# Kernel optimization log

Hardware: AMD Instinct MI355X
Metric: run time of the kernel (lower is better)

## Reference

```python
import jax, jax.numpy as jnp
import numpy as np

INPUT_SIZE = 32   # activity vocab
HIDDEN = 512
OUT = 33          # OUT-1 activity logits + 1 duration
COND = 128
LAYERS = 2
MAXLEN = 64
BATCH = 256
SOS = 0
SLOPE = 0.01      # LeakyReLU default negative slope

def _leaky(x):
    return jnp.where(x >= 0, x, SLOPE * x)

def setup_inputs() -> dict:
    key = jax.random.key(0)
    ks = jax.random.split(key, 16)
    s = 0.05  # small init scale keeps gates in a sane range
    return {
        "batch_size": BATCH,
        "h0": jax.random.normal(ks[0], (LAYERS, BATCH, HIDDEN), jnp.float32),
        "c0": jax.random.normal(ks[1], (LAYERS, BATCH, HIDDEN), jnp.float32),
        "conditionals": jax.random.normal(ks[2], (BATCH, COND), jnp.float32),
        "emb": jax.random.normal(ks[3], (INPUT_SIZE, HIDDEN - 1), jnp.float32) * s,
        "Wih": jax.random.normal(ks[4], (LAYERS, 4 * HIDDEN, HIDDEN), jnp.float32) * s,
        "Whh": jax.random.normal(ks[5], (LAYERS, 4 * HIDDEN, HIDDEN), jnp.float32) * s,
        "bih": jax.random.normal(ks[6], (LAYERS, 4 * HIDDEN), jnp.float32) * s,
        "bhh": jax.random.normal(ks[7], (LAYERS, 4 * HIDDEN), jnp.float32) * s,
        "fcW": jax.random.normal(ks[8], (HIDDEN, COND), jnp.float32) * s,
        "fcb": jax.random.normal(ks[9], (HIDDEN,), jnp.float32) * s,
        "fc2W": jax.random.normal(ks[10], (HIDDEN, HIDDEN), jnp.float32) * s,
        "fc2b": jax.random.normal(ks[11], (HIDDEN,), jnp.float32) * s,
        "fc3W": jax.random.normal(ks[12], (OUT, HIDDEN), jnp.float32) * s,
        "fc3b": jax.random.normal(ks[13], (OUT,), jnp.float32) * s,
    }

def reference(batch_size, h0, c0, conditionals, emb, Wih, Whh, bih, bhh,
              fcW, fcb, fc2W, fc2b, fc3W, fc3b):
    B = h0.shape[1]
    # conditionals branch is step-invariant: compute once (same math as per-step fc+LeakyReLU)
    cond = _leaky(conditionals @ fcW.T + fcb)  # [B, H]
    # decoder_input = zeros[B,1,2] with act channel = sos
    inp0 = jnp.concatenate(
        [jnp.full((B, 1), float(SOS), jnp.float32), jnp.zeros((B, 1), jnp.float32)], axis=-1)

    def step(carry, _):
        h, c, inp = carry  # h,c: [L,B,H], inp: [B,2]
        # CustomDurationEmbedding: embed act index, concat duration channel -> [B,H]
        x = jnp.concatenate([emb[inp[:, 0].astype(jnp.int32)], inp[:, 1:]], axis=-1)
        hs, cs = [], []
        for l in range(LAYERS):  # seq_len==1 per step -> one LSTM cell per layer
            g = x @ Wih[l].T + bih[l] + h[l] @ Whh[l].T + bhh[l]  # [B,4H]
            i_g, f_g, g_g, o_g = jnp.split(g, 4, axis=-1)         # torch gate order i,f,g,o
            c_l = jax.nn.sigmoid(f_g) * c[l] + jax.nn.sigmoid(i_g) * jnp.tanh(g_g)
            h_l = jax.nn.sigmoid(o_g) * jnp.tanh(c_l)
            hs.append(h_l); cs.append(c_l)
            x = h_l
        h_new, c_new = jnp.stack(hs), jnp.stack(cs)
        # conditional_add: (lstm_out + cond) -> fc2 -> LeakyReLU -> fc3
        pred = _leaky((x + cond) @ fc2W.T + fc2b) @ fc3W.T + fc3b  # [B,OUT]
        # pack: topk(1) over activity logits; softmax over singleton seq dim == 1.0
        act = jnp.argmax(pred[:, :OUT - 1], axis=-1).astype(pred.dtype)[:, None]
        dur = jnp.ones((B, 1), pred.dtype)
        nxt = jnp.concatenate([act, dur], axis=-1)
        return (h_new, c_new, nxt), pred

    _, outs = jax.lax.scan(step, (h0, c0, inp0), None, length=MAXLEN)  # [T,B,OUT]
    outs = jnp.transpose(outs, (1, 0, 2))  # [B,T,OUT]
    acts_log_probs = jax.nn.log_softmax(outs[..., :OUT - 1], axis=-1)
    durations = jax.nn.softmax(outs[..., OUT - 1:], axis=1)  # Softmax(dim=-2): over time
    return jnp.concatenate([acts_log_probs, durations], axis=-1)
```

## Files before the change

kernel.cpp:

```cpp
#include <hip/hip_runtime.h>
#include <math.h>

#define BB   256
#define HH   512
#define TT   64
#define NOUT 33
#define CD   128
#define NTHR 1024
#define NWG  256
#define LOFF (4*HH*HH)
#define SZ   (HH*BB)
#define FC2OFF 4194304

typedef float f16v __attribute__((ext_vector_type(16)));
typedef float f8v  __attribute__((ext_vector_type(8)));
typedef const __attribute__((address_space(4))) float cfloat;
typedef const __attribute__((address_space(4))) f16v  cf16v;
typedef const __attribute__((address_space(4))) f8v   cf8v;

__device__ __forceinline__ float sigm(float x)  { return 1.0f/(1.0f+expf(-x)); }
__device__ __forceinline__ float lrelu(float x) { return x >= 0.0f ? x : 0.01f*x; }

__device__ __forceinline__ float gld(const float* p) {
  return __hip_atomic_load(p, __ATOMIC_RELAXED, __HIP_MEMORY_SCOPE_AGENT);
}
__device__ __forceinline__ float2 gld2(const float* p) {
  unsigned long long v = __hip_atomic_load((const unsigned long long*)p,
                                           __ATOMIC_RELAXED, __HIP_MEMORY_SCOPE_AGENT);
  union { unsigned long long u; float2 f; } c; c.u = v; return c.f;
}
__device__ __forceinline__ void gst(float* p, float v) {
  __hip_atomic_store(p, v, __ATOMIC_RELAXED, __HIP_MEMORY_SCOPE_AGENT);
}
__device__ __forceinline__ unsigned gldu(const unsigned* p) {
  return __hip_atomic_load(p, __ATOMIC_RELAXED, __HIP_MEMORY_SCOPE_AGENT);
}

__device__ __forceinline__ cfloat* cptr(const float* p) {
  unsigned long long u = (unsigned long long)p;
  unsigned lo = __builtin_amdgcn_readfirstlane((unsigned)u);
  unsigned hi = __builtin_amdgcn_readfirstlane((unsigned)(u >> 32));
  return (cfloat*)((((unsigned long long)hi) << 32) | (unsigned long long)lo);
}

__device__ __forceinline__ void gbar(unsigned* bar, unsigned ep, int grp, bool fence) {
  __syncthreads();
  if (threadIdx.x == 0) {
    if (fence) __builtin_amdgcn_fence(__ATOMIC_RELEASE, "agent");
    unsigned old = __hip_atomic_fetch_add(&bar[grp*16], 1u, __ATOMIC_RELAXED, __HIP_MEMORY_SCOPE_AGENT);
    if (old == ep*32u + 31u) {
      unsigned o2 = __hip_atomic_fetch_add(&bar[128], 1u, __ATOMIC_RELAXED, __HIP_MEMORY_SCOPE_AGENT);
      if (o2 == ep*8u + 7u)
        __hip_atomic_store(&bar[144], ep+1u, __ATOMIC_RELAXED, __HIP_MEMORY_SCOPE_AGENT);
    }
    while (gldu(&bar[144]) < ep+1u) __builtin_amdgcn_s_sleep(1);
    if (fence) __builtin_amdgcn_fence(__ATOMIC_ACQUIRE, "agent");
  }
  __syncthreads();
}

extern "C" __global__ void __launch_bounds__(256)
transpose_weights(const float* __restrict__ Wih, const float* __restrict__ Whh,
                  const float* __restrict__ fc2W, float* __restrict__ wsT)
{
  const int i = blockIdx.x, tid = threadIdx.x;
  float* dst = wsT + (size_t)i*32768;
  #pragma unroll 1
  for (int idx = tid; idx < 32768; idx += 256) {
    int slot = idx & 31, k = (idx>>5)&511, l = idx>>14;
    int a = slot>>4, r = slot&15, u = r>>2, g = r&3;
    int hu = i*4 + u;
    const float* src = a ? Whh : Wih;
    dst[idx] = src[(size_t)l*LOFF + (size_t)(g*HH+hu)*HH + k];
  }
  float* dstf = wsT + FC2OFF + (size_t)i*2048;
  #pragma unroll 1
  for (int idx = tid; idx < 2048; idx += 256) {
    int r = idx & 3, k = idx >> 2;
    dstf[idx] = fc2W[(size_t)(i*4+r)*HH + k];
  }
}

__device__ __forceinline__ void lstm_phase(const float* __restrict__ wTl,
    const float* __restrict__ bias, float* __restrict__ red,
    const float* __restrict__ xsrc, const float* __restrict__ hsrc,
    float* __restrict__ hdst, float& creg, int i, int j, int tid)
{
  const int lane = tid & 63, ks = tid >> 6;
  cf16v* wp = (cf16v*)cptr(wTl + (size_t)(ks*32)*32);
  const int bo = j*128 + 2*lane;
  const float* xp = xsrc + (size_t)(ks*32)*BB + bo;
  const float* hp = hsrc + (size_t)(ks*32)*BB + bo;

  float acc[32];
  #pragma unroll
  for (int r = 0; r < 32; ++r) acc[r] = 0.f;

  float2 qx0, qh0, qx1, qh1, nx0, nh0, nx1, nh1;
  qx0 = gld2(xp);      qh0 = gld2(hp);
  qx1 = gld2(xp + BB); qh1 = gld2(hp + BB);

  #pragma unroll 1
  for (int it = 0; it < 16; ++it) {
    if (it+1 < 16) {
      nx0 = gld2(xp + (2*it+2)*BB); nh0 = gld2(hp + (2*it+2)*BB);
      nx1 = gld2(xp + (2*it+3)*BB); nh1 = gld2(hp + (2*it+3)*BB);
    }
    {
      f16v wi = wp[it*4+0], wh = wp[it*4+1];
      #pragma unroll
      for (int r = 0; r < 16; ++r) {
        acc[2*r]   += wi[r]*qx0.x + wh[r]*qh0.x;
        acc[2*r+1] += wi[r]*qx0.y + wh[r]*qh0.y;
      }
    }
    {
      f16v wi = wp[it*4+2], wh = wp[it*4+3];
      #pragma unroll
      for (int r = 0; r < 16; ++r) {
        acc[2*r]   += wi[r]*qx1.x + wh[r]*qh1.x;
        acc[2*r+1] += wi[r]*qx1.y + wh[r]*qh1.y;
      }
    }
    qx0 = nx0; qh0 = nh0; qx1 = nx1; qh1 = nh1;
  }
  #pragma unroll
  for (int r = 0; r < 16; ++r)
    *(float2*)(red + (size_t)(ks*16 + r)*128 + 2*lane) = make_float2(acc[2*r], acc[2*r+1]);
  __syncthreads();
  if (tid < 512) {
    const int lhu = tid >> 7, b = tid & 127;
    float g4[4];
    #pragma unroll
    for (int gg = 0; gg < 4; ++gg) {
      float s = bias[lhu*4+gg];
      #pragma unroll
      for (int q = 0; q < 16; ++q) s += red[(size_t)(q*16 + lhu*4+gg)*128 + b];
      g4[gg] = s;
    }
    float ig=sigm(g4[0]), fg=sigm(g4[1]), gv=tanhf(g4[2]), og=sigm(g4[3]);
    float cn = fg*creg + ig*gv;
    creg = cn;
    gst(hdst + (size_t)(i*4+lhu)*BB + j*128 + b, og*tanhf(cn));
  }
}

__device__ __forceinline__ void fc2_phase(const float* __restrict__ h2src,
    const float* __restrict__ wsTf, float* __restrict__ yb,
    const float* lds_bc, const float* condY_l, float* __restrict__ red,
    int i, int j, int tid)
{
  const int lane = tid & 63, ks = tid >> 6;
  cf8v* wpf = (cf8v*)cptr(wsTf + (size_t)ks*128);
  const int bo = j*128 + 2*lane;
  const float* hp = h2src + (size_t)(ks*32)*BB + bo;
  float acc[8];
  #pragma unroll
  for (int r = 0; r < 8; ++r) acc[r] = 0.f;
  float2 qh0, qh1, nh0, nh1;
  qh0 = gld2(hp); qh1 = gld2(hp + BB);
  #pragma unroll 1
  for (int it = 0; it < 16; ++it) {
    if (it+1 < 16) {
      nh0 = gld2(hp + (2*it+2)*BB);
      nh1 = gld2(hp + (2*it+3)*BB);
    }
    f8v w = wpf[it];
    #pragma unroll
    for (int r = 0; r < 4; ++r) {
      acc[2*r]   += w[r]*qh0.x + w[4+r]*qh1.x;
      acc[2*r+1] += w[r]*qh0.y + w[4+r]*qh1.y;
    }
    qh0 = nh0; qh1 = nh1;
  }
  #pragma unroll
  for (int r = 0; r < 4; ++r)
    *(float2*)(red + (size_t)(ks*4+r)*128 + 2*lane) = make_float2(acc[2*r], acc[2*r+1]);
  __syncthreads();
  if (tid < 512) {
    int r = tid >> 7, b = tid & 127;
    float s = lds_bc[r] + condY_l[r*128+b];
    #pragma unroll
    for (int q = 0; q < 16; ++q) s += red[(size_t)(q*4+r)*128 + b];
    gst(yb + (size_t)(i*4+r)*BB + j*128 + b, lrelu(s));
  }
}

extern "C" __global__ void __launch_bounds__(NTHR)
decoder_kernel(const float* __restrict__ h0, const float* __restrict__ c0,
               const float* __restrict__ conds, const float* __restrict__ emb,
               const float* __restrict__ wsTW, const float* __restrict__ bih,
               const float* __restrict__ bhh, const float* __restrict__ fcW,
               const float* __restrict__ fcb, const float* __restrict__ fc2W,
               const float* __restrict__ fc2b, const float* __restrict__ fc3W,
               const float* __restrict__ fc3b,
               float* __restrict__ out, unsigned* bar, float* wsf)
{
  const int w = blockIdx.x;
  const int i = w & 127, j = w >> 7;
  const int grp = w & 7;
  const int tid = threadIdx.x;

  float* xbuf  = wsf;
  float* h1a = wsf + 1*SZ;  float* h1b = wsf + 2*SZ;
  float* h2a = wsf + 3*SZ;  float* h2b = wsf + 4*SZ;
  float* yb  = wsf + 5*SZ;
  float* condb = wsf + 6*SZ;
  const float* wTi  = wsTW + (size_t)i*32768;
  const float* wsTf = wsTW + FC2OFF + (size_t)i*2048;

  __shared__ float red[32768];
  __shared__ float lds_y[HH];
  __shared__ float part[NOUT][17];
  __shared__ float condY_l[512];
  __shared__ float lds_b1[16], lds_b2[16], lds_bc[4];
  __shared__ int   lds_act;

  if (tid < 16) {
    int u2 = tid >> 2, g = tid & 3;
    int hu = i*4 + u2;
    lds_b1[tid] = bih[g*HH+hu] + bhh[g*HH+hu];
    lds_b2[tid] = bih[4*HH + g*HH+hu] + bhh[4*HH + g*HH+hu];
  }
  if (tid < 4) lds_bc[tid] = fc2b[i*4 + tid];

  {
    int u = tid >> 8, b = tid & 255;
    int hug = i*4 + u;
    h1a[(size_t)hug*BB + b] = h0[(size_t)b*HH + hug];
    h2a[(size_t)hug*BB + b] = h0[(size_t)(BB+b)*HH + hug];
    xbuf[(size_t)hug*BB + b] = (hug < HH-1) ? emb[hug] : 0.0f;
    const float* crow = conds + (size_t)b*CD;
    cfloat* fr = cptr(fcW + (size_t)hug*CD);
    float s = fcb[hug];
    #pragma unroll 4
    for (int q = 0; q < CD; q += 4)
      s += fr[q]*crow[q] + fr[q+1]*crow[q+1] + fr[q+2]*crow[q+2] + fr[q+3]*crow[q+3];
    condb[(size_t)hug*BB + b] = lrelu(s);
  }
  float c1 = 0.f, c2 = 0.f;
  if (tid < 512) {
    int lhu = tid >> 7, b = tid & 127;
    int hug = i*4 + lhu, bg = j*128 + b;
    c1 = c0[(size_t)bg*HH + hug];
    c2 = c0[(size_t)(BB+bg)*HH + hug];
  }
  unsigned ep = 0;
  gbar(bar, ep++, grp, true);

  if (tid < 512) {
    int r = tid >> 7, b = tid & 127, bg = j*128 + b;
    cfloat* wr = cptr(fc2W + (size_t)(i*4+r)*HH);
    float s = 0.f;
    #pragma unroll 4
    for (int k = 0; k < HH; ++k) s += wr[k]*condb[(size_t)k*BB + bg];
    condY_l[r*128 + b] = s;
  }
  __syncthreads();

  for (int t = 0; t < TT; ++t) {
    float* h1r = (t&1) ? h1b : h1a;  float* h1w = (t&1) ? h1a : h1b;
    float* h2r = (t&1) ? h2b : h2a;  float* h2w = (t&1) ? h2a : h2b;

    lstm_phase(wTi,         lds_b1, red, xbuf, h1r, h1w, c1, i, j, tid);
    gbar(bar, ep++, grp, false);
    lstm_phase(wTi + 16384, lds_b2, red, h1w, h2r, h2w, c2, i, j, tid);
    gbar(bar, ep++, grp, false);
    fc2_phase(h2w, wsTf, yb, lds_bc, condY_l, red, i, j, tid);
    gbar(bar, ep++, grp, false);
    {
      if (tid < 512) lds_y[tid] = gld(yb + (size_t)tid*BB + w);
      __syncthreads();
      int o = 0, kc = 0;
      bool active = false;
      if (tid < 512)      { o = tid & 31; kc = tid >> 5; active = true; }
      else if (tid < 528) { o = 32;       kc = tid - 512; active = true; }
      if (active) {
        float p = 0.f;
        const float* fw = fc3W + (size_t)o*HH + kc*32;
        #pragma unroll
        for (int k2 = 0; k2 < 32; ++k2) p += fw[k2] * lds_y[kc*32 + k2];
        part[o][kc] = p;
      }
      __syncthreads();
      float predv = -1e30f;
      if (tid < NOUT) {
        float s = fc3b[tid];
        #pragma unroll
        for (int kc2 = 0; kc2 < 16; ++kc2) s += part[tid][kc2];
        predv = s;
        out[(size_t)(w*TT + t)*NOUT + tid] = s;
      }
      if (tid < 64) {
        float v  = (tid < 32) ? predv : -1e30f;
        int  idx = tid;
        #pragma unroll
        for (int off = 32; off > 0; off >>= 1) {
          float ov = __shfl_xor(v, off);
          int   oi = __shfl_xor(idx, off);
          if (ov > v || (ov == v && oi < idx)) { v = ov; idx = oi; }
        }
        if (tid == 0) lds_act = idx;
      }
      __syncthreads();
      const int act = lds_act;
      if (tid < 512)
        gst(xbuf + (size_t)tid*BB + w, (tid < HH-1) ? emb[(size_t)act*(HH-1) + tid] : 1.0f);
    }
    gbar(bar, ep++, grp, false);
  }

  if (tid < TT) {
    const int s = tid;
    float* po = out + (size_t)(w*TT + s)*NOUT;
    float v[NOUT];
    #pragma unroll
    for (int o = 0; o < NOUT; ++o) v[o] = po[o];
    float m = v[0];
    #pragma unroll
    for (int o = 1; o < 32; ++o) m = fmaxf(m, v[o]);
    float sum = 0.f;
    #pragma unroll
    for (int o = 0; o < 32; ++o) sum += expf(v[o] - m);
    float lse = m + logf(sum);
    #pragma unroll
    for (int o = 0; o < 32; ++o) po[o] = v[o] - lse;
    float d = v[32];
    float dm = d;
    #pragma unroll
    for (int off = 32; off > 0; off >>= 1) dm = fmaxf(dm, __shfl_xor(dm, off));
    float e = expf(d - dm);
    float es = e;
    #pragma unroll
    for (int off = 32; off > 0; off >>= 1) es += __shfl_xor(es, off);
    po[32] = e / es;
  }
}

extern "C" void kernel_launch(void* const* d_in, const int* in_sizes, int n_in,
                              void* d_out, int out_size, void* d_ws, size_t ws_size,
                              hipStream_t stream) {
  const float* h0   = (const float*)d_in[1];
  const float* c0   = (const float*)d_in[2];
  const float* cnd  = (const float*)d_in[3];
  const float* emb  = (const float*)d_in[4];
  const float* Wih  = (const float*)d_in[5];
  const float* Whh  = (const float*)d_in[6];
  const float* bih  = (const float*)d_in[7];
  const float* bhh  = (const float*)d_in[8];
  const float* fcW  = (const float*)d_in[9];
  const float* fcb  = (const float*)d_in[10];
  const float* fc2W = (const float*)d_in[11];
  const float* fc2b = (const float*)d_in[12];
  const float* fc3W = (const float*)d_in[13];
  const float* fc3b = (const float*)d_in[14];

  unsigned* bar = (unsigned*)d_ws;
  float* wsf = (float*)((char*)d_ws + 1024);
  float* wsT = wsf + 7*SZ;

  (void)hipMemsetAsync(d_ws, 0, 1024, stream);

  hipLaunchKernelGGL(transpose_weights, dim3(128), dim3(256), 0, stream,
                     Wih, Whh, fc2W, wsT);
  hipLaunchKernelGGL(decoder_kernel, dim3(NWG), dim3(NTHR), 0, stream,
                     h0, c0, cnd, emb, wsT, bih, bhh, fcW, fcb,
                     fc2W, fc2b, fc3W, fc3b, (float*)d_out, bar, wsf);
}
```

Before: 4.062 ms.

## Split batch across 512 workgroups with independent per-batch-slice grid barriers

Doubles the persistent grid to 512 workgroups, each handling 64 batch columns instead of 128. The grid barrier becomes per batch quarter, so the four batch slices synchronise independently because batch rows never interact. Only half of the workgroups now run the fc3, argmax and embedding step, each for its own batch row. LSTM and fc2 inner loops switch from paired float2 loads to scalar loads with double-buffered prefetch, and gate accumulation goes through an extra LDS buffer. In exchange, each weight slice is read twice as often, and the persistent barrier scheme only works if two 1024-thread workgroups fit on each CU at the same time.

```diff
diff --git a/kernel.cpp b/kernel.cpp
--- a/kernel.cpp
+++ b/kernel.cpp
@@ -7,27 +7,20 @@
 #define NOUT 33
 #define CD   128
 #define NTHR 1024
-#define NWG  256
+#define NWG  512
 #define LOFF (4*HH*HH)
 #define SZ   (HH*BB)
 #define FC2OFF 4194304
 
 typedef float f16v __attribute__((ext_vector_type(16)));
-typedef float f8v  __attribute__((ext_vector_type(8)));
 typedef const __attribute__((address_space(4))) float cfloat;
 typedef const __attribute__((address_space(4))) f16v  cf16v;
-typedef const __attribute__((address_space(4))) f8v   cf8v;
 
 __device__ __forceinline__ float sigm(float x)  { return 1.0f/(1.0f+expf(-x)); }
 __device__ __forceinline__ float lrelu(float x) { return x >= 0.0f ? x : 0.01f*x; }
 
 __device__ __forceinline__ float gld(const float* p) {
   return __hip_atomic_load(p, __ATOMIC_RELAXED, __HIP_MEMORY_SCOPE_AGENT);
-}
-__device__ __forceinline__ float2 gld2(const float* p) {
-  unsigned long long v = __hip_atomic_load((const unsigned long long*)p,
-                                           __ATOMIC_RELAXED, __HIP_MEMORY_SCOPE_AGENT);
-  union { unsigned long long u; float2 f; } c; c.u = v; return c.f;
 }
 __device__ __forceinline__ void gst(float* p, float v) {
   __hip_atomic_store(p, v, __ATOMIC_RELAXED, __HIP_MEMORY_SCOPE_AGENT);
@@ -43,17 +36,17 @@
   return (cfloat*)((((unsigned long long)hi) << 32) | (unsigned long long)lo);
 }
 
-__device__ __forceinline__ void gbar(unsigned* bar, unsigned ep, int grp, bool fence) {
+__device__ __forceinline__ void gbar(unsigned* bar, unsigned ep, int j, int sg, bool fence) {
   __syncthreads();
   if (threadIdx.x == 0) {
     if (fence) __builtin_amdgcn_fence(__ATOMIC_RELEASE, "agent");
-    unsigned old = __hip_atomic_fetch_add(&bar[grp*16], 1u, __ATOMIC_RELAXED, __HIP_MEMORY_SCOPE_AGENT);
+    unsigned old = __hip_atomic_fetch_add(&bar[(j*4+sg)*16], 1u, __ATOMIC_RELAXED, __HIP_MEMORY_SCOPE_AGENT);
     if (old == ep*32u + 31u) {
-      unsigned o2 = __hip_atomic_fetch_add(&bar[128], 1u, __ATOMIC_RELAXED, __HIP_MEMORY_SCOPE_AGENT);
-      if (o2 == ep*8u + 7u)
-        __hip_atomic_store(&bar[144], ep+1u, __ATOMIC_RELAXED, __HIP_MEMORY_SCOPE_AGENT);
-    }
-    while (gldu(&bar[144]) < ep+1u) __builtin_amdgcn_s_sleep(1);
+      unsigned o2 = __hip_atomic_fetch_add(&bar[256 + j*16], 1u, __ATOMIC_RELAXED, __HIP_MEMORY_SCOPE_AGENT);
+      if (o2 == ep*4u + 3u)
+        __hip_atomic_store(&bar[320 + j*16], ep+1u, __ATOMIC_RELAXED, __HIP_MEMORY_SCOPE_AGENT);
+    }
+    while (gldu(&bar[320 + j*16]) < ep+1u) __builtin_amdgcn_s_sleep(1);
     if (fence) __builtin_amdgcn_fence(__ATOMIC_ACQUIRE, "agent");
   }
   __syncthreads();
@@ -82,66 +75,66 @@
 }
 
 __device__ __forceinline__ void lstm_phase(const float* __restrict__ wTl,
-    const float* __restrict__ bias, float* __restrict__ red,
+    const float* __restrict__ bias, float* __restrict__ red, float* __restrict__ gbuf,
     const float* __restrict__ xsrc, const float* __restrict__ hsrc,
     float* __restrict__ hdst, float& creg, int i, int j, int tid)
 {
   const int lane = tid & 63, ks = tid >> 6;
   cf16v* wp = (cf16v*)cptr(wTl + (size_t)(ks*32)*32);
-  const int bo = j*128 + 2*lane;
+  const int bo = j*64 + lane;
   const float* xp = xsrc + (size_t)(ks*32)*BB + bo;
   const float* hp = hsrc + (size_t)(ks*32)*BB + bo;
 
-  float acc[32];
-  #pragma unroll
-  for (int r = 0; r < 32; ++r) acc[r] = 0.f;
-
-  float2 qx0, qh0, qx1, qh1, nx0, nh0, nx1, nh1;
-  qx0 = gld2(xp);      qh0 = gld2(hp);
-  qx1 = gld2(xp + BB); qh1 = gld2(hp + BB);
-
-  #pragma unroll 1
-  for (int it = 0; it < 16; ++it) {
-    if (it+1 < 16) {
-      nx0 = gld2(xp + (2*it+2)*BB); nh0 = gld2(hp + (2*it+2)*BB);
-      nx1 = gld2(xp + (2*it+3)*BB); nh1 = gld2(hp + (2*it+3)*BB);
-    }
-    {
-      f16v wi = wp[it*4+0], wh = wp[it*4+1];
+  float acc[16];
+  #pragma unroll
+  for (int r = 0; r < 16; ++r) acc[r] = 0.f;
+
+  float qA[16], qB[16];
+  #pragma unroll
+  for (int kk = 0; kk < 8; ++kk) {
+    qA[kk*2]   = gld(xp + kk*BB);
+    qA[kk*2+1] = gld(hp + kk*BB);
+  }
+  #pragma unroll
+  for (int c = 0; c < 4; ++c) {
+    float* q = (c & 1) ? qB : qA;
+    float* p = (c & 1) ? qA : qB;
+    if (c < 3) {
       #pragma unroll
-      for (int r = 0; r < 16; ++r) {
-        acc[2*r]   += wi[r]*qx0.x + wh[r]*qh0.x;
-        acc[2*r+1] += wi[r]*qx0.y + wh[r]*qh0.y;
-      }
-    }
-    {
-      f16v wi = wp[it*4+2], wh = wp[it*4+3];
+      for (int kk = 0; kk < 8; ++kk) {
+        p[kk*2]   = gld(xp + (c*8+8+kk)*BB);
+        p[kk*2+1] = gld(hp + (c*8+8+kk)*BB);
+      }
+    }
+    #pragma unroll
+    for (int kk = 0; kk < 8; ++kk) {
+      f16v wi = wp[(c*8+kk)*2];
+      f16v wh = wp[(c*8+kk)*2+1];
+      float xv = q[kk*2], hv = q[kk*2+1];
       #pragma unroll
-      for (int r = 0; r < 16; ++r) {
-        acc[2*r]   += wi[r]*qx1.x + wh[r]*qh1.x;
-        acc[2*r+1] += wi[r]*qx1.y + wh[r]*qh1.y;
-      }
-    }
-    qx0 = nx0; qh0 = nh0; qx1 = nx1; qh1 = nh1;
-  }
-  #pragma unroll
-  for (int r = 0; r < 16; ++r)
-    *(float2*)(red + (size_t)(ks*16 + r)*128 + 2*lane) = make_float2(acc[2*r], acc[2*r+1]);
-  __syncthreads();
-  if (tid < 512) {
-    const int lhu = tid >> 7, b = tid & 127;
-    float g4[4];
-    #pragma unroll
-    for (int gg = 0; gg < 4; ++gg) {
-      float s = bias[lhu*4+gg];
-      #pragma unroll
-      for (int q = 0; q < 16; ++q) s += red[(size_t)(q*16 + lhu*4+gg)*128 + b];
-      g4[gg] = s;
-    }
-    float ig=sigm(g4[0]), fg=sigm(g4[1]), gv=tanhf(g4[2]), og=sigm(g4[3]);
-    float cn = fg*creg + ig*gv;
+      for (int r = 0; r < 16; ++r) acc[r] += wi[r]*xv + wh[r]*hv;
+    }
+  }
+  #pragma unroll
+  for (int r = 0; r < 16; ++r) red[(size_t)(ks*16 + r)*64 + lane] = acc[r];
+  __syncthreads();
+  {
+    const int row = tid >> 6, b = tid & 63;
+    float s = bias[row];
+    #pragma unroll
+    for (int q = 0; q < 16; ++q) s += red[(size_t)(q*16 + row)*64 + b];
+    gbuf[row*64 + b] = s;
+  }
+  __syncthreads();
+  if (tid < 256) {
+    const int lhu = tid >> 6, b = tid & 63;
+    float i_g = sigm(gbuf[(lhu*4+0)*64 + b]);
+    float f_g = sigm(gbuf[(lhu*4+1)*64 + b]);
+    float g_g = tanhf(gbuf[(lhu*4+2)*64 + b]);
+    float o_g = sigm(gbuf[(lhu*4+3)*64 + b]);
+    float cn = f_g*creg + i_g*g_g;
     creg = cn;
-    gst(hdst + (size_t)(i*4+lhu)*BB + j*128 + b, og*tanhf(cn));
+    gst(hdst + (size_t)(i*4+lhu)*BB + j*64 + b, o_g*tanhf(cn));
   }
 }
 
@@ -151,38 +144,41 @@
     int i, int j, int tid)
 {
   const int lane = tid & 63, ks = tid >> 6;
-  cf8v* wpf = (cf8v*)cptr(wsTf + (size_t)ks*128);
-  const int bo = j*128 + 2*lane;
+  cf16v* wp = (cf16v*)cptr(wsTf + (size_t)(ks*32)*4);
+  const int bo = j*64 + lane;
   const float* hp = h2src + (size_t)(ks*32)*BB + bo;
-  float acc[8];
-  #pragma unroll
-  for (int r = 0; r < 8; ++r) acc[r] = 0.f;
-  float2 qh0, qh1, nh0, nh1;
-  qh0 = gld2(hp); qh1 = gld2(hp + BB);
-  #pragma unroll 1
-  for (int it = 0; it < 16; ++it) {
-    if (it+1 < 16) {
-      nh0 = gld2(hp + (2*it+2)*BB);
-      nh1 = gld2(hp + (2*it+3)*BB);
-    }
-    f8v w = wpf[it];
-    #pragma unroll
-    for (int r = 0; r < 4; ++r) {
-      acc[2*r]   += w[r]*qh0.x + w[4+r]*qh1.x;
-      acc[2*r+1] += w[r]*qh0.y + w[4+r]*qh1.y;
-    }
-    qh0 = nh0; qh1 = nh1;
-  }
-  #pragma unroll
-  for (int r = 0; r < 4; ++r)
-    *(float2*)(red + (size_t)(ks*4+r)*128 + 2*lane) = make_float2(acc[2*r], acc[2*r+1]);
-  __syncthreads();
-  if (tid < 512) {
-    int r = tid >> 7, b = tid & 127;
-    float s = lds_bc[r] + condY_l[r*128+b];
-    #pragma unroll
-    for (int q = 0; q < 16; ++q) s += red[(size_t)(q*4+r)*128 + b];
-    gst(yb + (size_t)(i*4+r)*BB + j*128 + b, lrelu(s));
+  float acc[4] = {0.f, 0.f, 0.f, 0.f};
+  float qA[8], qB[8];
+  #pragma unroll
+  for (int kk = 0; kk < 8; ++kk) qA[kk] = gld(hp + kk*BB);
+  #pragma unroll
+  for (int c = 0; c < 4; ++c) {
+    float* q = (c & 1) ? qB : qA;
+    float* p = (c & 1) ? qA : qB;
+    if (c < 3) {
+      #pragma unroll
+      for (int kk = 0; kk < 8; ++kk) p[kk] = gld(hp + (c*8+8+kk)*BB);
+    }
+    #pragma unroll
+    for (int kk2 = 0; kk2 < 2; ++kk2) {
+      f16v wv = wp[c*2 + kk2];
+      #pragma unroll
+      for (int k4 = 0; k4 < 4; ++k4) {
+        float hv = q[kk2*4 + k4];
+        #pragma unroll
+        for (int r = 0; r < 4; ++r) acc[r] += wv[k4*4 + r]*hv;
+      }
+    }
+  }
+  #pragma unroll
+  for (int r = 0; r < 4; ++r) red[(size_t)(ks*4 + r)*64 + lane] = acc[r];
+  __syncthreads();
+  if (tid < 256) {
+    const int r = tid >> 6, b = tid & 63;
+    float s = lds_bc[r] + condY_l[r*64 + b];
+    #pragma unroll
+    for (int q = 0; q < 16; ++q) s += red[(size_t)(q*4 + r)*64 + b];
+    gst(yb + (size_t)(i*4+r)*BB + j*64 + b, lrelu(s));
   }
 }
 
@@ -198,10 +194,10 @@
 {
   const int w = blockIdx.x;
   const int i = w & 127, j = w >> 7;
-  const int grp = w & 7;
+  const int sg = (i >> 5) & 3;
   const int tid = threadIdx.x;
 
-  float* xbuf  = wsf;
+  float* xbuf = wsf;
   float* h1a = wsf + 1*SZ;  float* h1b = wsf + 2*SZ;
   float* h2a = wsf + 3*SZ;  float* h2b = wsf + 4*SZ;
   float* yb  = wsf + 5*SZ;
@@ -209,16 +205,17 @@
   const float* wTi  = wsTW + (size_t)i*32768;
   const float* wsTf = wsTW + FC2OFF + (size_t)i*2048;
 
-  __shared__ float red[32768];
+  __shared__ float red[16384];
+  __shared__ float gbuf[1024];
   __shared__ float lds_y[HH];
   __shared__ float part[NOUT][17];
-  __shared__ float condY_l[512];
+  __shared__ float condY_l[256];
   __shared__ float lds_b1[16], lds_b2[16], lds_bc[4];
   __shared__ int   lds_act;
 
   if (tid < 16) {
-    int u2 = tid >> 2, g = tid & 3;
-    int hu = i*4 + u2;
+    int u = tid >> 2, g = tid & 3;
+    int hu = i*4 + u;
     lds_b1[tid] = bih[g*HH+hu] + bhh[g*HH+hu];
     lds_b2[tid] = bih[4*HH + g*HH+hu] + bhh[4*HH + g*HH+hu];
   }
@@ -239,37 +236,40 @@
     condb[(size_t)hug*BB + b] = lrelu(s);
   }
   float c1 = 0.f, c2 = 0.f;
-  if (tid < 512) {
-    int lhu = tid >> 7, b = tid & 127;
-    int hug = i*4 + lhu, bg = j*128 + b;
+  if (tid < 256) {
+    int lhu = tid >> 6, b = tid & 63;
+    int hug = i*4 + lhu, bg = j*64 + b;
     c1 = c0[(size_t)bg*HH + hug];
     c2 = c0[(size_t)(BB+bg)*HH + hug];
   }
   unsigned ep = 0;
-  gbar(bar, ep++, grp, true);
-
-  if (tid < 512) {
-    int r = tid >> 7, b = tid & 127, bg = j*128 + b;
+  gbar(bar, ep++, j, sg, true);
+
+  if (tid < 256) {
+    int r = tid >> 6, b = tid & 63, bg = j*64 + b;
     cfloat* wr = cptr(fc2W + (size_t)(i*4+r)*HH);
     float s = 0.f;
     #pragma unroll 4
     for (int k = 0; k < HH; ++k) s += wr[k]*condb[(size_t)k*BB + bg];
-    condY_l[r*128 + b] = s;
-  }
-  __syncthreads();
+    condY_l[r*64 + b] = s;
+  }
+  __syncthreads();
+
+  const bool dOwner = (i < 64);
+  const int  drow   = j*64 + i;
 
   for (int t = 0; t < TT; ++t) {
     float* h1r = (t&1) ? h1b : h1a;  float* h1w = (t&1) ? h1a : h1b;
     float* h2r = (t&1) ? h2b : h2a;  float* h2w = (t&1) ? h2a : h2b;
 
-    lstm_phase(wTi,         lds_b1, red, xbuf, h1r, h1w, c1, i, j, tid);
-    gbar(bar, ep++, grp, false);
-    lstm_phase(wTi + 16384, lds_b2, red, h1w, h2r, h2w, c2, i, j, tid);
-    gbar(bar, ep++, grp, false);
+    lstm_phase(wTi,         lds_b1, red, gbuf, xbuf, h1r, h1w, c1, i, j, tid);
+    gbar(bar, ep++, j, sg, false);
+    lstm_phase(wTi + 16384, lds_b2, red, gbuf, h1w, h2r, h2w, c2, i, j, tid);
+    gbar(bar, ep++, j, sg, false);
     fc2_phase(h2w, wsTf, yb, lds_bc, condY_l, red, i, j, tid);
-    gbar(bar, ep++, grp, false);
-    {
-      if (tid < 512) lds_y[tid] = gld(yb + (size_t)tid*BB + w);
+    gbar(bar, ep++, j, sg, false);
+    if (dOwner) {
+      if (tid < 512) lds_y[tid] = gld(yb + (size_t)tid*BB + drow);
       __syncthreads();
       int o = 0, kc = 0;
       bool active = false;
@@ -289,7 +289,7 @@
         #pragma unroll
         for (int kc2 = 0; kc2 < 16; ++kc2) s += part[tid][kc2];
         predv = s;
-        out[(size_t)(w*TT + t)*NOUT + tid] = s;
+        out[(size_t)(drow*TT + t)*NOUT + tid] = s;
       }
       if (tid < 64) {
         float v  = (tid < 32) ? predv : -1e30f;
@@ -305,14 +305,14 @@
       __syncthreads();
       const int act = lds_act;
       if (tid < 512)
-        gst(xbuf + (size_t)tid*BB + w, (tid < HH-1) ? emb[(size_t)act*(HH-1) + tid] : 1.0f);
-    }
-    gbar(bar, ep++, grp, false);
-  }
-
-  if (tid < TT) {
+        gst(xbuf + (size_t)tid*BB + drow, (tid < HH-1) ? emb[(size_t)act*(HH-1) + tid] : 1.0f);
+    }
+    gbar(bar, ep++, j, sg, false);
+  }
+
+  if (dOwner && tid < TT) {
     const int s = tid;
-    float* po = out + (size_t)(w*TT + s)*NOUT;
+    float* po = out + (size_t)(drow*TT + s)*NOUT;
     float v[NOUT];
     #pragma unroll
     for (int o = 0; o < NOUT; ++o) v[o] = po[o];
@@ -356,10 +356,10 @@
   const float* fc3b = (const float*)d_in[14];
 
   unsigned* bar = (unsigned*)d_ws;
-  float* wsf = (float*)((char*)d_ws + 1024);
+  float* wsf = (float*)((char*)d_ws + 4096);
   float* wsT = wsf + 7*SZ;
 
-  (void)hipMemsetAsync(d_ws, 0, 1024, stream);
+  (void)hipMemsetAsync(d_ws, 0, 4096, stream);
 
   hipLaunchKernelGGL(transpose_weights, dim3(128), dim3(256), 0, stream,
                      Wih, Whh, fc2W, wsT);
```

After: 11.22 ms. 176% more time.
